# Kernel optimization log

Hardware: AMD Instinct MI355X
Metric: run time of the kernel (lower is better)

## Reference

```python
import jax, jax.numpy as jnp
import numpy as np

NUM_HEADS = 32
NUM_KV_HEADS = 8
HEAD_DIM = 64
Q_MULT = NUM_HEADS // NUM_KV_HEADS  # 4
WINDOW = 128
BATCH = 2
SEQ = 2048


def setup_inputs() -> dict:
    key = jax.random.key(0)
    k1, k2, k3 = jax.random.split(key, 3)
    Q = jax.random.normal(k1, (BATCH, SEQ, NUM_HEADS * HEAD_DIM), dtype=jnp.float32)
    K = jax.random.normal(k2, (BATCH, SEQ, NUM_KV_HEADS * HEAD_DIM), dtype=jnp.float32)
    V = jax.random.normal(k3, (BATCH, SEQ, NUM_KV_HEADS * HEAD_DIM), dtype=jnp.float32)
    sinks = jnp.zeros((NUM_HEADS,), dtype=jnp.float32)
    return {"Q": Q, "K": K, "V": V, "sinks": sinks}


def _sdpa_single(Qb, Kb, Vb, sinks):
    # Qb: (n, num_heads*head_dim); Kb/Vb: (n, num_kv_heads*head_dim)
    n = Qb.shape[0]
    Q = Qb.reshape(n, NUM_KV_HEADS, Q_MULT, HEAD_DIM)
    K = Kb.reshape(n, NUM_KV_HEADS, HEAD_DIM)
    V = Vb.reshape(n, NUM_KV_HEADS, HEAD_DIM)
    sm_scale = 1.0 / np.sqrt(HEAD_DIM)
    # NOTE: the reference torch sdpa() builds S (sinks) but never adds it to QK;
    # we faithfully reproduce that (sinks unused in the math).
    q_idx = jnp.arange(n)[:, None]
    k_idx = jnp.arange(n)[None, :]
    # causal AND within sliding window of 128
    allowed = (k_idx <= q_idx) & (k_idx > q_idx - WINDOW)
    mask = jnp.where(allowed, jnp.float32(0.0), -jnp.inf)
    # scores: (h, m, q, k) where h = kv head, m = q_mult (GQA expand of K is implicit via einsum)
    QK = jnp.einsum('qhmd,khd->hmqk', Q, K) * sm_scale + mask[None, None, :, :]
    W = jax.nn.softmax(QK, axis=-1)
    attn = jnp.einsum('hmqk,khd->qhmd', W, V)
    return attn.reshape(n, -1)


def reference(Q, K, V, sinks):
    return jax.vmap(_sdpa_single, in_axes=(0, 0, 0, None))(Q, K, V, sinks)
```

## Files before the change

kernel.cpp:

```cpp
#include <hip/hip_runtime.h>


constexpr int NKV = 8, QM = 4, WIN = 128, BATCH = 2, SEQ = 2048;
constexpr int QSTRIDE = 2048, KSTRIDE = 512, HD = 64;

typedef __attribute__((ext_vector_type(8))) __bf16 bf16x8;
typedef __attribute__((ext_vector_type(8))) short short8_t;
typedef __attribute__((ext_vector_type(4))) float f32x4;
typedef __attribute__((ext_vector_type(4))) unsigned int uint4_t;

__device__ __forceinline__ unsigned pk2(float lo, float hi) {
    return __builtin_amdgcn_perm(__float_as_uint(hi), __float_as_uint(lo), 0x07060302u);
}
__device__ __forceinline__ short8_t pack8(float4 a, float4 b) {
    return __builtin_bit_cast(short8_t,
        (uint4_t){pk2(a.x, a.y), pk2(a.z, a.w), pk2(b.x, b.y), pk2(b.z, b.w)});
}
__device__ __forceinline__ short hi16(float f) {
    return (short)(__float_as_uint(f) >> 16);
}

__device__ __forceinline__ f32x4 mfma16(short8_t a, short8_t b, f32x4 c) {
    return __builtin_amdgcn_mfma_f32_16x16x32_bf16(
        __builtin_bit_cast(bf16x8, a), __builtin_bit_cast(bf16x8, b), c, 0, 0, 0);
}

constexpr float C1f = 0.18033688011112042f;
constexpr float C0f = -11.541560327111707f;

__global__ __launch_bounds__(256, 4)
void swa_mfma9(const float* __restrict__ Q, const float* __restrict__ K,
               const float* __restrict__ V, float* __restrict__ O)
{
    __shared__ __align__(16) short Ksh[32][72];
    __shared__ __align__(16) short Vsh[64][40];
    __shared__ __align__(16) short Psh[4][16][40];

    const int tid  = threadIdx.x;
    const int lane = tid & 63;
    const int w    = tid >> 6;
    const int col  = lane & 15;
    const int quad = lane >> 4;

    int blk = blockIdx.x;
    const int b   = blk & 1;
    const int kvh = (blk >> 1) & 7;
    const int qg  = blk >> 4;
    const int q0  = qg * 32;
    const int h   = kvh * QM + w;

    const float* QA = Q + ((size_t)(b * SEQ + q0 + col) * QSTRIDE + h * HD);
    const float* QB = QA + (size_t)16 * QSTRIDE;
    short8_t aqA0, aqA1, aqB0, aqB1;
    {
        float4 f0 = *(const float4*)(QA + quad * 8);
        float4 f1 = *(const float4*)(QA + quad * 8 + 4);
        float4 g0 = *(const float4*)(QA + 32 + quad * 8);
        float4 g1 = *(const float4*)(QA + 32 + quad * 8 + 4);
        aqA0 = pack8(f0, f1);
        aqA1 = pack8(g0, g1);
        f0 = *(const float4*)(QB + quad * 8);
        f1 = *(const float4*)(QB + quad * 8 + 4);
        g0 = *(const float4*)(QB + 32 + quad * 8);
        g1 = *(const float4*)(QB + 32 + quad * 8 + 4);
        aqB0 = pack8(f0, f1);
        aqB1 = pack8(g0, g1);
    }

    const float* Kb = K + ((size_t)b * SEQ * KSTRIDE + (size_t)kvh * HD);
    const float* Vb = V + ((size_t)b * SEQ * KSTRIDE + (size_t)kvh * HD);

    f32x4 oA0 = {0.f,0.f,0.f,0.f}, oA1 = oA0, oA2 = oA0, oA3 = oA0;
    f32x4 oB0 = oA0, oB1 = oA0, oB2 = oA0, oB3 = oA0;
    float liA[4] = {0.f,0.f,0.f,0.f}, liB[4] = {0.f,0.f,0.f,0.f};

    const int krow = tid >> 3, kseg = tid & 7;
    const int vd = tid & 63, vkg = tid >> 6;

    const int t_start = (q0 >= WIN) ? 0 : ((WIN - q0) >> 5);

#pragma unroll 1
    for (int t = t_start; t < 5; ++t) {
        const int kbase = q0 - WIN + 32 * t;

        __syncthreads();
        {
            const float* s = Kb + (size_t)(kbase + krow) * KSTRIDE + kseg * 8;
            const float4 a = *(const float4*)s;
            const float4 c = *(const float4*)(s + 4);
            *(short8_t*)&Ksh[krow][kseg * 8] = pack8(a, c);
        }
        {
            const float* sv = Vb + (size_t)(kbase + vkg * 8) * KSTRIDE + vd;
            const float u0 = sv[0],           u1 = sv[KSTRIDE],     u2 = sv[2*KSTRIDE],
                        u3 = sv[3*KSTRIDE],   u4 = sv[4*KSTRIDE],   u5 = sv[5*KSTRIDE],
                        u6 = sv[6*KSTRIDE],   u7 = sv[7*KSTRIDE];
            *(short8_t*)&Vsh[vd][vkg * 8] = __builtin_bit_cast(short8_t,
                (uint4_t){pk2(u0, u1), pk2(u2, u3), pk2(u4, u5), pk2(u6, u7)});
        }
        __syncthreads();

        const short8_t b0lo = *(const short8_t*)&Ksh[col][quad * 8];
        const short8_t b0hi = *(const short8_t*)&Ksh[col][quad * 8 + 32];
        const short8_t b1lo = *(const short8_t*)&Ksh[16 + col][quad * 8];
        const short8_t b1hi = *(const short8_t*)&Ksh[16 + col][quad * 8 + 32];
        const short8_t vb0  = *(const short8_t*)&Vsh[col][quad * 8];
        const short8_t vb1  = *(const short8_t*)&Vsh[16 + col][quad * 8];
        const short8_t vb2  = *(const short8_t*)&Vsh[32 + col][quad * 8];
        const short8_t vb3  = *(const short8_t*)&Vsh[48 + col][quad * 8];

        {
            f32x4 s0 = {0.f,0.f,0.f,0.f}, s1 = s0;
            s0 = mfma16(aqA0, b0lo, s0); s0 = mfma16(aqA1, b0hi, s0);
            if (t < 4) { s1 = mfma16(aqA0, b1lo, s1); s1 = mfma16(aqA1, b1hi, s1); }
#pragma unroll
            for (int r = 0; r < 4; ++r) {
                const int rr = quad * 4 + r;
                float a0 = fmaf(s0[r], C1f, C0f);
                float a1 = fmaf(s1[r], C1f, C0f);
                if (t == 0) a0 = (col > rr)  ? a0 : -1e30f;
                if (t == 4) { a0 = (col <= rr) ? a0 : -1e30f; a1 = -1e30f; }
                const float p0 = exp2f(a0);
                const float p1 = (t < 4) ? exp2f(a1) : 0.f;
                liA[r] += p0 + p1;
                Psh[w][rr][col]      = hi16(p0);
                Psh[w][rr][16 + col] = hi16(p1);
            }
            const short8_t pa = *(const short8_t*)&Psh[w][col][quad * 8];
            oA0 = mfma16(pa, vb0, oA0); oA1 = mfma16(pa, vb1, oA1);
            oA2 = mfma16(pa, vb2, oA2); oA3 = mfma16(pa, vb3, oA3);
        }

        {
            f32x4 s0 = {0.f,0.f,0.f,0.f}, s1 = s0;
            if (t > 0) { s0 = mfma16(aqB0, b0lo, s0); s0 = mfma16(aqB1, b0hi, s0); }
            s1 = mfma16(aqB0, b1lo, s1); s1 = mfma16(aqB1, b1hi, s1);
#pragma unroll
            for (int r = 0; r < 4; ++r) {
                const int rr = quad * 4 + r;
                float a0 = fmaf(s0[r], C1f, C0f);
                float a1 = fmaf(s1[r], C1f, C0f);
                if (t == 0) a1 = (col > rr) ? a1 : -1e30f;
                if (t == 4) a1 = (col <= rr) ? a1 : -1e30f;
                const float p0 = (t > 0) ? exp2f(a0) : 0.f;
                const float p1 = exp2f(a1);
                liB[r] += p0 + p1;
                Psh[w][rr][col]      = hi16(p0);
                Psh[w][rr][16 + col] = hi16(p1);
            }
            const short8_t pa = *(const short8_t*)&Psh[w][col][quad * 8];
            oB0 = mfma16(pa, vb0, oB0); oB1 = mfma16(pa, vb1, oB1);
            oB2 = mfma16(pa, vb2, oB2); oB3 = mfma16(pa, vb3, oB3);
        }
    }

    float* OA = O + ((size_t)(b * SEQ + q0) * QSTRIDE + h * HD);
    float* OB = OA + (size_t)16 * QSTRIDE;
#pragma unroll
    for (int r = 0; r < 4; ++r) {
        float lA = liA[r], lB = liB[r];
        lA += __shfl_xor(lA, 1); lA += __shfl_xor(lA, 2);
        lA += __shfl_xor(lA, 4); lA += __shfl_xor(lA, 8);
        lB += __shfl_xor(lB, 1); lB += __shfl_xor(lB, 2);
        lB += __shfl_xor(lB, 4); lB += __shfl_xor(lB, 8);
        const float iA = 1.0f / lA, iB = 1.0f / lB;
        const size_t row = (size_t)(quad * 4 + r) * QSTRIDE;
        OA[row + col]      = oA0[r] * iA;
        OA[row + 16 + col] = oA1[r] * iA;
        OA[row + 32 + col] = oA2[r] * iA;
        OA[row + 48 + col] = oA3[r] * iA;
        OB[row + col]      = oB0[r] * iB;
        OB[row + 16 + col] = oB1[r] * iB;
        OB[row + 32 + col] = oB2[r] * iB;
        OB[row + 48 + col] = oB3[r] * iB;
    }
}

extern "C" void kernel_launch(void* const* d_in, const int* in_sizes, int n_in,
                              void* d_out, int out_size, void* d_ws, size_t ws_size,
                              hipStream_t stream) {
    const float* Q = (const float*)d_in[0];
    const float* K = (const float*)d_in[1];
    const float* V = (const float*)d_in[2];
    float* O = (float*)d_out;

    dim3 grid(BATCH * NKV * (SEQ / 32));
    dim3 block(256);
    swa_mfma9<<<grid, block, 0, stream>>>(Q, K, V, O);
}
```

Measured before the change: 104.1 us.

## Double-buffer K/V shared tiles and prefetch next tile during compute

Splits the K and V shared-memory tiles into two buffers. The next 32-key tile's global loads are issued in the middle of the current tile's MFMA and softmax work, then stored into the alternate buffer, so each iteration needs only one barrier. This is meant to hide global load latency behind compute, at the cost of doubled LDS use for K/V and more live registers, which could reduce occupancy.

```diff
diff --git a/kernel.cpp b/kernel.cpp
--- a/kernel.cpp
+++ b/kernel.cpp
@@ -29,11 +29,11 @@
 constexpr float C0f = -11.541560327111707f;
 
 __global__ __launch_bounds__(256, 4)
-void swa_mfma9(const float* __restrict__ Q, const float* __restrict__ K,
-               const float* __restrict__ V, float* __restrict__ O)
+void swa_mfma10(const float* __restrict__ Q, const float* __restrict__ K,
+                const float* __restrict__ V, float* __restrict__ O)
 {
-    __shared__ __align__(16) short Ksh[32][72];
-    __shared__ __align__(16) short Vsh[64][40];
+    __shared__ __align__(16) short Ksh[2][32][72];
+    __shared__ __align__(16) short Vsh[2][64][40];
     __shared__ __align__(16) short Psh[4][16][40];
 
     const int tid  = threadIdx.x;
@@ -79,35 +79,43 @@
 
     const int t_start = (q0 >= WIN) ? 0 : ((WIN - q0) >> 5);
 
+    {
+        const int kbase = q0 - WIN + 32 * t_start;
+        const float* s = Kb + (size_t)(kbase + krow) * KSTRIDE + kseg * 8;
+        const float4 a = *(const float4*)s;
+        const float4 c = *(const float4*)(s + 4);
+        *(short8_t*)&Ksh[0][krow][kseg * 8] = pack8(a, c);
+        const float* sv = Vb + (size_t)(kbase + vkg * 8) * KSTRIDE + vd;
+        const float u0 = sv[0],         u1 = sv[KSTRIDE],   u2 = sv[2*KSTRIDE],
+                    u3 = sv[3*KSTRIDE], u4 = sv[4*KSTRIDE], u5 = sv[5*KSTRIDE],
+                    u6 = sv[6*KSTRIDE], u7 = sv[7*KSTRIDE];
+        *(short8_t*)&Vsh[0][vd][vkg * 8] = __builtin_bit_cast(short8_t,
+            (uint4_t){pk2(u0, u1), pk2(u2, u3), pk2(u4, u5), pk2(u6, u7)});
+    }
+
+    int cur = 0;
 #pragma unroll 1
     for (int t = t_start; t < 5; ++t) {
-        const int kbase = q0 - WIN + 32 * t;
+        const int nkbase = q0 - WIN + 32 * t + 32;
+        const bool pf = (t < 4);
 
         __syncthreads();
-        {
-            const float* s = Kb + (size_t)(kbase + krow) * KSTRIDE + kseg * 8;
-            const float4 a = *(const float4*)s;
-            const float4 c = *(const float4*)(s + 4);
-            *(short8_t*)&Ksh[krow][kseg * 8] = pack8(a, c);
-        }
-        {
-            const float* sv = Vb + (size_t)(kbase + vkg * 8) * KSTRIDE + vd;
-            const float u0 = sv[0],           u1 = sv[KSTRIDE],     u2 = sv[2*KSTRIDE],
-                        u3 = sv[3*KSTRIDE],   u4 = sv[4*KSTRIDE],   u5 = sv[5*KSTRIDE],
-                        u6 = sv[6*KSTRIDE],   u7 = sv[7*KSTRIDE];
-            *(short8_t*)&Vsh[vd][vkg * 8] = __builtin_bit_cast(short8_t,
-                (uint4_t){pk2(u0, u1), pk2(u2, u3), pk2(u4, u5), pk2(u6, u7)});
-        }
-        __syncthreads();
-
-        const short8_t b0lo = *(const short8_t*)&Ksh[col][quad * 8];
-        const short8_t b0hi = *(const short8_t*)&Ksh[col][quad * 8 + 32];
-        const short8_t b1lo = *(const short8_t*)&Ksh[16 + col][quad * 8];
-        const short8_t b1hi = *(const short8_t*)&Ksh[16 + col][quad * 8 + 32];
-        const short8_t vb0  = *(const short8_t*)&Vsh[col][quad * 8];
-        const short8_t vb1  = *(const short8_t*)&Vsh[16 + col][quad * 8];
-        const short8_t vb2  = *(const short8_t*)&Vsh[32 + col][quad * 8];
-        const short8_t vb3  = *(const short8_t*)&Vsh[48 + col][quad * 8];
+
+        const short8_t b0lo = *(const short8_t*)&Ksh[cur][col][quad * 8];
+        const short8_t b0hi = *(const short8_t*)&Ksh[cur][col][quad * 8 + 32];
+        const short8_t b1lo = *(const short8_t*)&Ksh[cur][16 + col][quad * 8];
+        const short8_t b1hi = *(const short8_t*)&Ksh[cur][16 + col][quad * 8 + 32];
+        const short8_t vb0  = *(const short8_t*)&Vsh[cur][col][quad * 8];
+        const short8_t vb1  = *(const short8_t*)&Vsh[cur][16 + col][quad * 8];
+        const short8_t vb2  = *(const short8_t*)&Vsh[cur][32 + col][quad * 8];
+        const short8_t vb3  = *(const short8_t*)&Vsh[cur][48 + col][quad * 8];
+
+        float4 nka = {0.f,0.f,0.f,0.f}, nkc = nka;
+        if (pf) {
+            const float* s = Kb + (size_t)(nkbase + krow) * KSTRIDE + kseg * 8;
+            nka = *(const float4*)s;
+            nkc = *(const float4*)(s + 4);
+        }
 
         {
             f32x4 s0 = {0.f,0.f,0.f,0.f}, s1 = s0;
@@ -131,6 +139,16 @@
             oA2 = mfma16(pa, vb2, oA2); oA3 = mfma16(pa, vb3, oA3);
         }
 
+        float nu0 = 0.f, nu1 = 0.f, nu2 = 0.f, nu3 = 0.f,
+              nu4 = 0.f, nu5 = 0.f, nu6 = 0.f, nu7 = 0.f;
+        if (pf) {
+            *(short8_t*)&Ksh[cur ^ 1][krow][kseg * 8] = pack8(nka, nkc);
+            const float* sv = Vb + (size_t)(nkbase + vkg * 8) * KSTRIDE + vd;
+            nu0 = sv[0];           nu1 = sv[KSTRIDE];     nu2 = sv[2*KSTRIDE];
+            nu3 = sv[3*KSTRIDE];   nu4 = sv[4*KSTRIDE];   nu5 = sv[5*KSTRIDE];
+            nu6 = sv[6*KSTRIDE];   nu7 = sv[7*KSTRIDE];
+        }
+
         {
             f32x4 s0 = {0.f,0.f,0.f,0.f}, s1 = s0;
             if (t > 0) { s0 = mfma16(aqB0, b0lo, s0); s0 = mfma16(aqB1, b0hi, s0); }
@@ -152,6 +170,12 @@
             oB0 = mfma16(pa, vb0, oB0); oB1 = mfma16(pa, vb1, oB1);
             oB2 = mfma16(pa, vb2, oB2); oB3 = mfma16(pa, vb3, oB3);
         }
+
+        if (pf) {
+            *(short8_t*)&Vsh[cur ^ 1][vd][vkg * 8] = __builtin_bit_cast(short8_t,
+                (uint4_t){pk2(nu0, nu1), pk2(nu2, nu3), pk2(nu4, nu5), pk2(nu6, nu7)});
+        }
+        cur ^= 1;
     }
 
     float* OA = O + ((size_t)(b * SEQ + q0) * QSTRIDE + h * HD);
@@ -186,5 +210,5 @@
 
     dim3 grid(BATCH * NKV * (SEQ / 32));
     dim3 block(256);
-    swa_mfma9<<<grid, block, 0, stream>>>(Q, K, V, O);
-}
+    swa_mfma10<<<grid, block, 0, stream>>>(Q, K, V, O);
+}
```

Measured after the change: 109.0 us. 1.05x slower.

## Process two 32-row query groups per block to share K/V tile loads

Applied to the files above, without the earlier changes.

Doubles the block to 512 threads covering 64 query rows, with two warp groups offset by one K/V tile sharing a sliding 6-tile stream. Each K/V tile is loaded and converted once per block and reused by both query groups, and the K and V loads are split across the two thread halves instead of done by every thread. This cuts global K/V traffic and conversion work per query, at the cost of one extra loop iteration where half the warps sit idle, and half as many blocks in the grid.

```diff
diff --git a/kernel.cpp b/kernel.cpp
--- a/kernel.cpp
+++ b/kernel.cpp
@@ -28,17 +28,19 @@
 constexpr float C1f = 0.18033688011112042f;
 constexpr float C0f = -11.541560327111707f;
 
-__global__ __launch_bounds__(256, 4)
-void swa_mfma9(const float* __restrict__ Q, const float* __restrict__ K,
-               const float* __restrict__ V, float* __restrict__ O)
+__global__ __launch_bounds__(512, 4)
+void swa_mfma13(const float* __restrict__ Q, const float* __restrict__ K,
+                const float* __restrict__ V, float* __restrict__ O)
 {
     __shared__ __align__(16) short Ksh[32][72];
     __shared__ __align__(16) short Vsh[64][40];
-    __shared__ __align__(16) short Psh[4][16][40];
+    __shared__ __align__(16) short Psh[8][16][40];
 
     const int tid  = threadIdx.x;
     const int lane = tid & 63;
     const int w    = tid >> 6;
+    const int m    = w & 3;
+    const int grp  = w >> 2;
     const int col  = lane & 15;
     const int quad = lane >> 4;
 
@@ -46,10 +48,11 @@
     const int b   = blk & 1;
     const int kvh = (blk >> 1) & 7;
     const int qg  = blk >> 4;
-    const int q0  = qg * 32;
-    const int h   = kvh * QM + w;
+    const int q0  = qg * 64;
+    const int qb  = q0 + grp * 32;
+    const int h   = kvh * QM + m;
 
-    const float* QA = Q + ((size_t)(b * SEQ + q0 + col) * QSTRIDE + h * HD);
+    const float* QA = Q + ((size_t)(b * SEQ + qb + col) * QSTRIDE + h * HD);
     const float* QB = QA + (size_t)16 * QSTRIDE;
     short8_t aqA0, aqA1, aqB0, aqB1;
     {
@@ -75,22 +78,22 @@
     float liA[4] = {0.f,0.f,0.f,0.f}, liB[4] = {0.f,0.f,0.f,0.f};
 
     const int krow = tid >> 3, kseg = tid & 7;
-    const int vd = tid & 63, vkg = tid >> 6;
+    const int vt = tid & 255, vd = vt & 63, vkg = vt >> 6;
 
-    const int t_start = (q0 >= WIN) ? 0 : ((WIN - q0) >> 5);
+    const int tsA = (q0 >= WIN) ? 0 : ((WIN - q0) >> 5);
+    const int tsw = (qb >= WIN) ? 0 : ((WIN - qb) >> 5);
 
 #pragma unroll 1
-    for (int t = t_start; t < 5; ++t) {
+    for (int t = tsA; t < 6; ++t) {
         const int kbase = q0 - WIN + 32 * t;
 
         __syncthreads();
-        {
+        if (tid < 256) {
             const float* s = Kb + (size_t)(kbase + krow) * KSTRIDE + kseg * 8;
             const float4 a = *(const float4*)s;
             const float4 c = *(const float4*)(s + 4);
             *(short8_t*)&Ksh[krow][kseg * 8] = pack8(a, c);
-        }
-        {
+        } else {
             const float* sv = Vb + (size_t)(kbase + vkg * 8) * KSTRIDE + vd;
             const float u0 = sv[0],           u1 = sv[KSTRIDE],     u2 = sv[2*KSTRIDE],
                         u3 = sv[3*KSTRIDE],   u4 = sv[4*KSTRIDE],   u5 = sv[5*KSTRIDE],
@@ -99,6 +102,9 @@
                 (uint4_t){pk2(u0, u1), pk2(u2, u3), pk2(u4, u5), pk2(u6, u7)});
         }
         __syncthreads();
+
+        const int tl = t - grp;
+        if (tl < tsw || tl > 4) continue;
 
         const short8_t b0lo = *(const short8_t*)&Ksh[col][quad * 8];
         const short8_t b0hi = *(const short8_t*)&Ksh[col][quad * 8 + 32];
@@ -112,16 +118,16 @@
         {
             f32x4 s0 = {0.f,0.f,0.f,0.f}, s1 = s0;
             s0 = mfma16(aqA0, b0lo, s0); s0 = mfma16(aqA1, b0hi, s0);
-            if (t < 4) { s1 = mfma16(aqA0, b1lo, s1); s1 = mfma16(aqA1, b1hi, s1); }
+            if (tl < 4) { s1 = mfma16(aqA0, b1lo, s1); s1 = mfma16(aqA1, b1hi, s1); }
 #pragma unroll
             for (int r = 0; r < 4; ++r) {
                 const int rr = quad * 4 + r;
                 float a0 = fmaf(s0[r], C1f, C0f);
                 float a1 = fmaf(s1[r], C1f, C0f);
-                if (t == 0) a0 = (col > rr)  ? a0 : -1e30f;
-                if (t == 4) { a0 = (col <= rr) ? a0 : -1e30f; a1 = -1e30f; }
+                if (tl == 0) a0 = (col > rr)  ? a0 : -1e30f;
+                if (tl == 4) { a0 = (col <= rr) ? a0 : -1e30f; a1 = -1e30f; }
                 const float p0 = exp2f(a0);
-                const float p1 = (t < 4) ? exp2f(a1) : 0.f;
+                const float p1 = (tl < 4) ? exp2f(a1) : 0.f;
                 liA[r] += p0 + p1;
                 Psh[w][rr][col]      = hi16(p0);
                 Psh[w][rr][16 + col] = hi16(p1);
@@ -133,16 +139,16 @@
 
         {
             f32x4 s0 = {0.f,0.f,0.f,0.f}, s1 = s0;
-            if (t > 0) { s0 = mfma16(aqB0, b0lo, s0); s0 = mfma16(aqB1, b0hi, s0); }
+            if (tl > 0) { s0 = mfma16(aqB0, b0lo, s0); s0 = mfma16(aqB1, b0hi, s0); }
             s1 = mfma16(aqB0, b1lo, s1); s1 = mfma16(aqB1, b1hi, s1);
 #pragma unroll
             for (int r = 0; r < 4; ++r) {
                 const int rr = quad * 4 + r;
                 float a0 = fmaf(s0[r], C1f, C0f);
                 float a1 = fmaf(s1[r], C1f, C0f);
-                if (t == 0) a1 = (col > rr) ? a1 : -1e30f;
-                if (t == 4) a1 = (col <= rr) ? a1 : -1e30f;
-                const float p0 = (t > 0) ? exp2f(a0) : 0.f;
+                if (tl == 0) a1 = (col > rr) ? a1 : -1e30f;
+                if (tl == 4) a1 = (col <= rr) ? a1 : -1e30f;
+                const float p0 = (tl > 0) ? exp2f(a0) : 0.f;
                 const float p1 = exp2f(a1);
                 liB[r] += p0 + p1;
                 Psh[w][rr][col]      = hi16(p0);
@@ -154,7 +160,7 @@
         }
     }
 
-    float* OA = O + ((size_t)(b * SEQ + q0) * QSTRIDE + h * HD);
+    float* OA = O + ((size_t)(b * SEQ + qb) * QSTRIDE + h * HD);
     float* OB = OA + (size_t)16 * QSTRIDE;
 #pragma unroll
     for (int r = 0; r < 4; ++r) {
@@ -184,7 +190,7 @@
     const float* V = (const float*)d_in[2];
     float* O = (float*)d_out;
 
-    dim3 grid(BATCH * NKV * (SEQ / 32));
-    dim3 block(256);
-    swa_mfma9<<<grid, block, 0, stream>>>(Q, K, V, O);
+    dim3 grid(BATCH * NKV * (SEQ / 64));
+    dim3 block(512);
+    swa_mfma13<<<grid, block, 0, stream>>>(Q, K, V, O);
 }
```

Measured after the change: 111.5 us. 1.07x slower.
